# Kernel tuning notes

Measured on AMD Instinct MI355X. Metric: run time of the kernel, lower is better.

Reference implementation:

```python
import jax, jax.numpy as jnp
import numpy as np

S = 10        # spiking_segment_count
TEMP = 50.0

def setup_inputs() -> dict:
    key = jax.random.key(0)
    ks = jax.random.split(key, 6)
    bs, din, dout = 2048, 1024, 1024
    x = jax.random.normal(ks[0], (bs, din), dtype=jnp.float32)
    t = jax.random.uniform(ks[1], (bs,), dtype=jnp.float32)  # in [0,1) subset of [-1,1]
    scale = 1.0 / np.sqrt(din)
    param_W = jax.random.normal(ks[2], (din, dout * S * 3), dtype=jnp.float32) * scale
    param_b = jax.random.normal(ks[3], (dout * S * 3,), dtype=jnp.float32) * 0.01
    norm_W = jax.random.normal(ks[4], (din, dout), dtype=jnp.float32) * scale
    norm_b = jax.random.normal(ks[5], (dout,), dtype=jnp.float32) * 0.01
    return {"x": x, "t": t, "param_W": param_W, "param_b": param_b,
            "norm_W": norm_W, "norm_b": norm_b}

def reference(x, t, param_W, param_b, norm_W, norm_b):
    bs = x.shape[0]
    dout = norm_W.shape[1]
    # param GEMM -> (bs, S, dout, 3)
    params = (x @ param_W + param_b).reshape(bs, S, dout, 3)
    weights = jax.nn.softmax(params[..., 0], axis=1)                 # (bs, S, dout)
    keypoints = jnp.concatenate(
        [jnp.zeros_like(weights[:, :1]), jnp.cumsum(weights, axis=1)], axis=1
    ) * 2.0 - 1.0                                                    # (bs, S+1, dout)
    slopes = jnp.tanh(params[..., 1])
    intercepts = params[..., 2]
    tt = t.reshape(-1, 1, 1)                                         # (bs, 1, 1)
    starts = keypoints[:, :S]
    ends = keypoints[:, 1:]
    residual = slopes * tt + intercepts                              # (bs, S, dout)
    validity = ((tt >= starts) & (tt < ends)) | ((tt == 1.0) & (ends == 1.0))
    vf = validity.astype(x.dtype)
    left_margin = jnp.sum((tt - starts) * vf, axis=1)                # (bs, dout)
    right_margin = jnp.sum((ends - tt) * vf, axis=1)
    lw = jax.nn.sigmoid(-TEMP * left_margin)
    rw = jax.nn.sigmoid(-TEMP * right_margin)
    lv = jnp.concatenate([vf[:, :1], vf[:, :-1]], axis=1)
    rv = jnp.concatenate([vf[:, 1:], vf[:, -1:]], axis=1)
    sw = -(lw + rw - 1.0)
    result = (lw * jnp.sum(residual * lv, axis=1)
              + sw * jnp.sum(residual * vf, axis=1)
              + rw * jnp.sum(residual * rv, axis=1))
    # norm == 'constant': subtract segment-wise integral, add norm_net(x)
    integral = jnp.sum(0.5 * slopes * (ends * ends - starts * starts)
                       + intercepts * weights, axis=1) * 0.5
    norm_target = x @ norm_W + norm_b
    return result - integral + norm_target
```

## Files before the change

### kernel.cpp

```cpp
#include <hip/hip_runtime.h>
#include <cstdint>
#include <cstddef>

#define BS    2048
#define DIN   1024
#define DOUT  1024
#define SSEG  10
#define NPAR  30720
#define NPK   20480
#define NCOL2 21504
#define NLG   10240
#define TAU   5e-5f
#define WL_CAP 1048576u

#define NB_SPLIT 2048
#define NB_NORM  1024
#define NB_TRW   2560

#define GEMM_BLKS 992

typedef _Float16 half_t;
typedef __attribute__((ext_vector_type(8))) _Float16 half8;
typedef __attribute__((ext_vector_type(4))) _Float16 half4;
typedef __attribute__((ext_vector_type(2))) _Float16 half2v;
typedef __attribute__((ext_vector_type(4))) float   floatx4;

__device__ __forceinline__ void gload16(const void* g, void* l) {
  __builtin_amdgcn_global_load_lds(
      (const __attribute__((address_space(1))) void*)g,
      (__attribute__((address_space(3))) void*)l, 16, 0, 0);
}

__global__ void k_zero(unsigned* c) { if (threadIdx.x == 0) *c = 0; }

__global__ __launch_bounds__(256) void k_prep(const float* __restrict__ x,
                                              half_t* __restrict__ xh,
                                              half_t* __restrict__ xl,
                                              const float* __restrict__ nW,
                                              const float* __restrict__ pW,
                                              half_t* __restrict__ wsm,
                                              half_t* __restrict__ wh,
                                              half_t* __restrict__ wlo,
                                              float* __restrict__ wlt,
                                              unsigned* __restrict__ cnt) {
  __shared__ float tile[32][384];
  int bid = blockIdx.x;
  int tid = threadIdx.x;

  if (bid < NB_SPLIT) {
    if (bid == 0 && tid == 0) *cnt = 0;
    int i = bid * 256 + tid;
    floatx4 v = ((const floatx4*)x)[i];
    half4 h, l;
    #pragma unroll
    for (int c = 0; c < 4; c++) { h[c] = (half_t)v[c]; l[c] = (half_t)(v[c] - (float)h[c]); }
    ((half4*)xh)[i] = h;
    ((half4*)xl)[i] = l;
    return;
  }

  if (bid < NB_SPLIT + NB_NORM) {
    int b2 = bid - NB_SPLIT;
    int col0 = (b2 & 31) * 32;
    int k0   = (b2 >> 5) * 32;
    int tx = tid & 31;
    int ty = tid >> 5;
    float* t33 = &tile[0][0];
    #pragma unroll
    for (int r = ty; r < 32; r += 8)
      t33[r * 33 + tx] = nW[(size_t)(k0 + r) * DOUT + col0 + tx];
    __syncthreads();
    #pragma unroll
    for (int r = ty; r < 32; r += 8)
      wsm[(size_t)(col0 + r + NPK) * DIN + k0 + tx] = (half_t)t33[tx * 33 + r];
    return;
  }

  int b3 = bid - NB_SPLIT - NB_NORM;
  int bx = b3 % 80;
  int k0 = (b3 / 80) * 32;
  int s  = bx >> 3;
  int d0 = (bx & 7) * 128;

  const float* sb = pW + (size_t)k0 * NPAR + bx * 384;
  for (int i = tid; i < 32 * 96; i += 256) {
    int r = i / 96, q = i - r * 96;
    ((floatx4*)&tile[r][0])[q] = ((const floatx4*)(sb + (size_t)r * NPAR))[q];
  }
  __syncthreads();

  for (int ci = tid; ci < 3072; ci += 256) {
    if (ci < 1024) {
      int rl = ci >> 2, kc = ci & 3;
      int jj = rl >> 1, cbit = rl & 1;
      int col = 3 * jj + 1 + cbit;
      half8 v;
      #pragma unroll
      for (int m = 0; m < 8; m++) v[m] = (half_t)tile[kc * 8 + m][col];
      *(half8*)(wsm + (size_t)(s * 2048 + 2 * (d0 + jj) + cbit) * DIN + k0 + kc * 8) = v;
    } else if (ci < 1536) {
      int u = ci - 1024;
      int jj = u >> 2, kc = u & 3;
      half8 v;
      #pragma unroll
      for (int m = 0; m < 8; m++) v[m] = (half_t)(tile[kc * 8 + m][3 * jj] * 32.0f);
      *(half8*)(wh + (size_t)(s * 1024 + d0 + jj) * DIN + k0 + kc * 8) = v;
    } else if (ci < 2048) {
      int u = ci - 1536;
      int jj = u >> 2, kc = u & 3;
      half8 v;
      #pragma unroll
      for (int m = 0; m < 8; m++) {
        float raw = tile[kc * 8 + m][3 * jj] * 32.0f;
        half_t h = (half_t)raw;
        v[m] = (half_t)(raw - (float)h);
      }
      *(half8*)(wlo + (size_t)(s * 1024 + d0 + jj) * DIN + k0 + kc * 8) = v;
    } else {
      int u = ci - 2048;
      int jj = u >> 3, kc = u & 7;
      floatx4 v;
      #pragma unroll
      for (int m = 0; m < 4; m++) v[m] = tile[kc * 4 + m][3 * jj];
      *(floatx4*)(wlt + (size_t)(s * 1024 + d0 + jj) * DIN + k0 + kc * 4) = v;
    }
  }
}

__global__ __launch_bounds__(512, 2) void k_gemm2(
    const half_t* __restrict__ xh, const half_t* __restrict__ xl,
    const half_t* __restrict__ wh, const half_t* __restrict__ wlo,
    const half_t* __restrict__ wsm,
    float* __restrict__ Lg, half_t* __restrict__ P,
    const float* __restrict__ pb, const float* __restrict__ nb) {
  __shared__ __attribute__((aligned(128))) char lds[131072];
  char* ldsA = lds;
  char* ldsB = lds + 65536;

  int bid = blockIdx.x;
  int tid = threadIdx.x;
  int w = tid >> 6, l = tid & 63;
  int wr = w >> 2, wc = w & 3;
  int l15 = l & 15, quad = l >> 4;

  int mode, mt, nt, KT;
  const half_t *A0, *A1, *A2, *B0, *B1, *B2;
  if (bid < 320) {
    int s = (bid & 7) * 40 + (bid >> 3);
    mode = 0; mt = s & 7; nt = s >> 3; KT = 96;
    A0 = xh; A1 = xl; A2 = xh; B0 = wh; B1 = wh; B2 = wlo;
  } else {
    int s2 = bid - 320;
    int s = (s2 & 7) * 84 + (s2 >> 3);
    mode = 1; mt = s & 7; nt = s >> 3; KT = 32;
    A0 = xh; A1 = xh; A2 = xh; B0 = wsm; B1 = wsm; B2 = wsm;
  }
  int m0 = mt * 256, n0 = nt * 256;

  int sp = (l & 7) ^ ((l >> 3) & 7);
  int srowA = m0 + w * 32 + 2 * (l >> 3) + (sp >> 2);
  int srowB = n0 + w * 32 + 2 * (l >> 3) + (sp >> 2);
  int scol = (sp & 3) * 8;

  int lofs = (l15 >> 1) * 128 + (((((l15 & 1) << 2) | quad) ^ (l15 >> 1)) << 4);
  const char* pA = ldsA + wr * 8192 + lofs;
  const char* pB = ldsB + wc * 4096 + lofs;

  auto stA = [&](int kt) {
    const half_t* As = (kt < 32) ? A0 : ((kt < 64) ? A1 : A2);
    const half_t* g = As + (size_t)srowA * DIN + (kt & 31) * 32 + scol;
    char* lb = ldsA + (kt & 3) * 16384 + w * 2048;
    gload16(g, lb);
    gload16(g + 16 * DIN, lb + 1024);
  };
  auto stB = [&](int kt) {
    const half_t* Bs = (kt < 32) ? B0 : ((kt < 64) ? B1 : B2);
    const half_t* g = Bs + (size_t)srowB * DIN + (kt & 31) * 32 + scol;
    char* lb = ldsB + (kt & 3) * 16384 + w * 2048;
    gload16(g, lb);
    gload16(g + 16 * DIN, lb + 1024);
  };

  floatx4 acc[8][4] = {};

  stA(0); stB(0); stA(1); stB(1); stA(2); stB(2);
  asm volatile("s_waitcnt vmcnt(8)" ::: "memory");
  __builtin_amdgcn_s_barrier();

  for (int kt = 0; kt < KT; ++kt) {
    const char* a = pA + (kt & 3) * 16384;
    const char* b = pB + (kt & 3) * 16384;
    half8 af[4], bf[4];
    #pragma unroll
    for (int ni = 0; ni < 4; ni++) bf[ni] = *(const half8*)(b + ni * 1024);
    #pragma unroll
    for (int mi = 0; mi < 4; mi++) af[mi] = *(const half8*)(a + mi * 1024);
    if (kt + 3 < KT) stA(kt + 3);
    __builtin_amdgcn_s_barrier();
    asm volatile("s_waitcnt lgkmcnt(0)" ::: "memory");
    __builtin_amdgcn_sched_barrier(0);
    __builtin_amdgcn_s_setprio(1);
    #pragma unroll
    for (int mi = 0; mi < 4; mi++)
      #pragma unroll
      for (int ni = 0; ni < 4; ni++)
        acc[mi][ni] = __builtin_amdgcn_mfma_f32_16x16x32_f16(af[mi], bf[ni], acc[mi][ni], 0, 0, 0);
    __builtin_amdgcn_s_setprio(0);
    __builtin_amdgcn_s_barrier();

    #pragma unroll
    for (int mi = 0; mi < 4; mi++) af[mi] = *(const half8*)(a + 4096 + mi * 1024);
    if (kt + 3 < KT) stB(kt + 3);
    __builtin_amdgcn_s_barrier();
    asm volatile("s_waitcnt lgkmcnt(0)" ::: "memory");
    __builtin_amdgcn_sched_barrier(0);
    __builtin_amdgcn_s_setprio(1);
    #pragma unroll
    for (int mi = 0; mi < 4; mi++)
      #pragma unroll
      for (int ni = 0; ni < 4; ni++)
        acc[4 + mi][ni] = __builtin_amdgcn_mfma_f32_16x16x32_f16(af[mi], bf[ni], acc[4 + mi][ni], 0, 0, 0);
    __builtin_amdgcn_s_setprio(0);
    if (kt < KT - 3)       { asm volatile("s_waitcnt vmcnt(8)" ::: "memory"); }
    else if (kt == KT - 3) { asm volatile("s_waitcnt vmcnt(4)" ::: "memory"); }
    else if (kt == KT - 2) { asm volatile("s_waitcnt vmcnt(0)" ::: "memory"); }
    __builtin_amdgcn_s_barrier();
  }

  int rbase = m0 + wr * 128 + quad * 4;
  int cbase = n0 + wc * 64 + l15;
  if (mode == 0) {
    #pragma unroll
    for (int ni = 0; ni < 4; ni++) {
      int col = cbase + ni * 16;
      float bias = pb[(col >> 10) * 3072 + (col & 1023) * 3];
      #pragma unroll
      for (int mi = 0; mi < 8; mi++) {
        int row = rbase + mi * 16;
        floatx4 v = acc[mi][ni];
        #pragma unroll
        for (int r = 0; r < 4; r++)
          Lg[(size_t)(row + r) * NLG + col] = v[r] * 0.03125f + bias;
      }
    }
  } else {
    #pragma unroll
    for (int ni = 0; ni < 4; ni++) {
      int col = cbase + ni * 16;
      float bias;
      if (col < NPK) {
        int s = col >> 11, rem = col & 2047;
        bias = pb[s * 3072 + 3 * (rem >> 1) + 1 + (rem & 1)];
      } else {
        bias = nb[col - NPK];
      }
      #pragma unroll
      for (int mi = 0; mi < 8; mi++) {
        int row = rbase + mi * 16;
        floatx4 v = acc[mi][ni];
        #pragma unroll
        for (int r = 0; r < 4; r++)
          P[(size_t)(row + r) * NCOL2 + col] = (half_t)(v[r] + bias);
      }
    }
  }
}

__device__ __forceinline__ float spiking_eval(const float* p, float tt, float* mind) {
  float mx = -1e30f;
  #pragma unroll
  for (int s = 0; s < SSEG; s++) mx = fmaxf(mx, p[3 * s]);
  float ew[10], wsum = 0.0f;
  #pragma unroll
  for (int s = 0; s < SSEG; s++) { ew[s] = __expf(p[3 * s] - mx); wsum += ew[s]; }
  float inv = 1.0f / wsum;

  float kp[11];
  kp[0] = -1.0f;
  float cum = 0.0f, md = 1e30f;
  #pragma unroll
  for (int s = 0; s < SSEG; s++) {
    cum += ew[s] * inv;
    kp[s + 1] = cum * 2.0f - 1.0f;
    md = fminf(md, fabsf(tt - kp[s + 1]));
  }
  *mind = md;

  float vf[10], resid[10];
  float lm = 0.0f, rm = 0.0f, integ = 0.0f;
  #pragma unroll
  for (int s = 0; s < SSEG; s++) {
    float p1 = p[3 * s + 1], p2 = p[3 * s + 2];
    float e2 = __expf(2.0f * fabsf(p1));
    float th = copysignf(1.0f - 2.0f / (e2 + 1.0f), p1);
    resid[s] = th * tt + p2;
    float st = kp[s], en = kp[s + 1];
    bool v = ((tt >= st) && (tt < en)) || ((tt == 1.0f) && (en == 1.0f));
    float vv = v ? 1.0f : 0.0f;
    vf[s] = vv;
    lm += (tt - st) * vv;
    rm += (en - tt) * vv;
    integ += 0.5f * th * (en * en - st * st) + p2 * (ew[s] * inv);
  }
  float resLV = 0.0f, resV = 0.0f, resRV = 0.0f;
  #pragma unroll
  for (int s = 0; s < SSEG; s++) {
    float lv = (s == 0) ? vf[0] : vf[s - 1];
    float rv = (s == 9) ? vf[9] : vf[s + 1];
    resLV += resid[s] * lv;
    resV  += resid[s] * vf[s];
    resRV += resid[s] * rv;
  }
  float lw = 1.0f / (1.0f + __expf(50.0f * lm));
  float rw = 1.0f / (1.0f + __expf(50.0f * rm));
  float swt = 1.0f - lw - rw;
  return lw * resLV + swt * resV + rw * resRV - 0.5f * integ + p[30];
}

__global__ __launch_bounds__(256) void k_pointwise(const half_t* __restrict__ P,
                                                   const float* __restrict__ Lg,
                                                   const float* __restrict__ t,
                                                   float* __restrict__ out,
                                                   unsigned* __restrict__ cnt,
                                                   unsigned* __restrict__ wl,
                                                   unsigned cap) {
  __shared__ __attribute__((aligned(16))) half_t sp[SSEG * 512];
  int b = blockIdx.x, dg = blockIdx.y, tid = threadIdx.x;
  const half_t* Pb = P + (size_t)b * NCOL2;
  for (int i = tid; i < SSEG * 64; i += 256) {
    int s = i >> 6, e = i & 63;
    ((uint4*)sp)[(s << 6) + e] = ((const uint4*)(Pb + s * 2048 + dg * 512))[e];
  }
  float tt = t[b];
  float nt = (float)Pb[NPK + dg * 256 + tid];
  const float* Lb = Lg + (size_t)b * NLG + dg * 256 + tid;
  __syncthreads();

  float p[31];
  #pragma unroll
  for (int s = 0; s < SSEG; s++) {
    p[3 * s] = Lb[s * 1024];
    half2v hv = ((const half2v*)sp)[s * 256 + tid];
    p[3 * s + 1] = (float)hv.x;
    p[3 * s + 2] = (float)hv.y;
  }
  p[30] = nt;
  float mind;
  float r = spiking_eval(p, tt, &mind);
  int d = dg * 256 + tid;
  out[(size_t)b * DOUT + d] = r;
  if (wl != nullptr && mind < TAU) {
    unsigned idx = atomicAdd(cnt, 1u);
    if (idx < cap) wl[idx] = ((unsigned)b << 10) | (unsigned)d;
  }
}

__global__ __launch_bounds__(256) void k_naive(const float* __restrict__ x,
                                               const float* __restrict__ t,
                                               const float* __restrict__ pW,
                                               const float* __restrict__ pb,
                                               const float* __restrict__ nW,
                                               const float* __restrict__ nb,
                                               float* __restrict__ out,
                                               unsigned* __restrict__ cnt,
                                               unsigned* __restrict__ wl,
                                               unsigned cap) {
  __shared__ float xs[DIN];
  int b = blockIdx.x, dg = blockIdx.y, tid = threadIdx.x;
  for (int i = tid; i < DIN; i += 256) xs[i] = x[(size_t)b * DIN + i];
  __syncthreads();
  int d = dg * 256 + tid;
  float acc[31];
  #pragma unroll
  for (int i = 0; i < 31; i++) acc[i] = 0.0f;
  for (int k = 0; k < DIN; k++) {
    float xv = xs[k];
    const float* wr = pW + (size_t)k * NPAR + 3 * d;
    #pragma unroll
    for (int s = 0; s < SSEG; s++) {
      acc[3 * s]     += xv * wr[s * 3072];
      acc[3 * s + 1] += xv * wr[s * 3072 + 1];
      acc[3 * s + 2] += xv * wr[s * 3072 + 2];
    }
    acc[30] += xv * nW[(size_t)k * DOUT + d];
  }
  #pragma unroll
  for (int s = 0; s < SSEG; s++) {
    acc[3 * s]     += pb[s * 3072 + 3 * d];
    acc[3 * s + 1] += pb[s * 3072 + 3 * d + 1];
    acc[3 * s + 2] += pb[s * 3072 + 3 * d + 2];
  }
  acc[30] += nb[d];
  float mind;
  float r = spiking_eval(acc, t[b], &mind);
  out[(size_t)b * DOUT + d] = r;
  if (wl != nullptr && mind < TAU) {
    unsigned idx = atomicAdd(cnt, 1u);
    if (idx < cap) wl[idx] = ((unsigned)b << 10) | (unsigned)d;
  }
}

__global__ __launch_bounds__(256) void k_redo(const float* __restrict__ x,
                                              const float* __restrict__ t,
                                              const float* __restrict__ pW,
                                              const float* __restrict__ pb,
                                              const float* __restrict__ nW,
                                              const float* __restrict__ nb,
                                              const half_t* __restrict__ P,
                                              const float* __restrict__ WLt,
                                              int haveP,
                                              const unsigned* __restrict__ cnt,
                                              const unsigned* __restrict__ wl,
                                              unsigned cap,
                                              float* __restrict__ out) {
  unsigned n = *cnt;
  if (n > cap) n = cap;
  int lane = threadIdx.x & 63;
  unsigned wave = (blockIdx.x * 256 + threadIdx.x) >> 6;
  unsigned nwaves = (gridDim.x * 256) >> 6;

  for (unsigned e = wave; e < n; e += nwaves) {
    unsigned code = wl[e];
    int b = (int)(code >> 10), d = (int)(code & 1023);

    double lg[10], sl[10], ic[10], nt = 0.0;
    #pragma unroll
    for (int s = 0; s < SSEG; s++) { lg[s] = 0.0; sl[s] = 0.0; ic[s] = 0.0; }

    if (haveP) {
      for (int k = lane; k < DIN; k += 64) {
        double xv = (double)x[(size_t)b * DIN + k];
        #pragma unroll
        for (int s = 0; s < SSEG; s++)
          lg[s] += xv * (double)WLt[(size_t)(s * 1024 + d) * DIN + k];
      }
    } else {
      for (int k = lane; k < DIN; k += 64) {
        double xv = (double)x[(size_t)b * DIN + k];
        const float* wr = pW + (size_t)k * NPAR + 3 * d;
        #pragma unroll
        for (int s = 0; s < SSEG; s++) {
          lg[s] += xv * (double)wr[s * 3072];
          sl[s] += xv * (double)wr[s * 3072 + 1];
          ic[s] += xv * (double)wr[s * 3072 + 2];
        }
        nt += xv * (double)nW[(size_t)k * DOUT + d];
      }
    }
    #pragma unroll
    for (int off = 32; off > 0; off >>= 1) {
      #pragma unroll
      for (int s = 0; s < SSEG; s++) lg[s] += __shfl_down(lg[s], off);
      if (!haveP) {
        #pragma unroll
        for (int s = 0; s < SSEG; s++) {
          sl[s] += __shfl_down(sl[s], off);
          ic[s] += __shfl_down(ic[s], off);
        }
        nt += __shfl_down(nt, off);
      }
    }

    if (lane == 0) {
      double slope[10], icpt[10], ntv;
      if (haveP) {
        const half_t* Pr = P + (size_t)b * NCOL2;
        #pragma unroll
        for (int s = 0; s < SSEG; s++) {
          slope[s] = tanh((double)(float)Pr[s * 2048 + 2 * d]);
          icpt[s]  = (double)(float)Pr[s * 2048 + 2 * d + 1];
        }
        ntv = (double)(float)Pr[NPK + d];
      } else {
        #pragma unroll
        for (int s = 0; s < SSEG; s++) {
          slope[s] = tanh(sl[s] + (double)pb[s * 3072 + 3 * d + 1]);
          icpt[s]  = ic[s] + (double)pb[s * 3072 + 3 * d + 2];
        }
        ntv = nt + (double)nb[d];
      }
      #pragma unroll
      for (int s = 0; s < SSEG; s++) lg[s] += (double)pb[s * 3072 + 3 * d];

      double mx = -1e300;
      #pragma unroll
      for (int s = 0; s < SSEG; s++) mx = fmax(mx, lg[s]);
      double ew[10], ws = 0.0;
      #pragma unroll
      for (int s = 0; s < SSEG; s++) { ew[s] = exp(lg[s] - mx); ws += ew[s]; }

      double kp[11];
      kp[0] = -1.0;
      double cum = 0.0;
      #pragma unroll
      for (int s = 0; s < SSEG; s++) { cum += ew[s] / ws; kp[s + 1] = cum * 2.0 - 1.0; }

      double tt = (double)t[b];
      double vf[10], resid[10], lm = 0.0, rm = 0.0, integ = 0.0;
      #pragma unroll
      for (int s = 0; s < SSEG; s++) {
        double st = kp[s], en = kp[s + 1];
        bool v = ((tt >= st) && (tt < en)) || ((tt == 1.0) && (en == 1.0));
        double vv = v ? 1.0 : 0.0;
        vf[s] = vv;
        resid[s] = slope[s] * tt + icpt[s];
        lm += (tt - st) * vv;
        rm += (en - tt) * vv;
        integ += 0.5 * slope[s] * (en * en - st * st) + icpt[s] * (ew[s] / ws);
      }
      double rLV = 0.0, rV = 0.0, rRV = 0.0;
      #pragma unroll
      for (int s = 0; s < SSEG; s++) {
        double lv = (s == 0) ? vf[0] : vf[s - 1];
        double rv = (s == 9) ? vf[9] : vf[s + 1];
        rLV += resid[s] * lv;
        rV  += resid[s] * vf[s];
        rRV += resid[s] * rv;
      }
      double lw = 1.0 / (1.0 + exp(50.0 * lm));
      double rw = 1.0 / (1.0 + exp(50.0 * rm));
      double res = lw * rLV + (1.0 - lw - rw) * rV + rw * rRV - 0.5 * integ + ntv;
      out[(size_t)b * DOUT + d] = (float)res;
    }
  }
}

extern "C" void kernel_launch(void* const* d_in, const int* in_sizes, int n_in,
                              void* d_out, int out_size, void* d_ws, size_t ws_size,
                              hipStream_t stream) {
  const float* x  = (const float*)d_in[0];
  const float* t  = (const float*)d_in[1];
  const float* pW = (const float*)d_in[2];
  const float* pb = (const float*)d_in[3];
  const float* nW = (const float*)d_in[4];
  const float* nb = (const float*)d_in[5];
  float* out = (float*)d_out;

  const size_t o_cnt = 0;
  const size_t o_wl  = 64;
  const size_t o_xh  = o_wl  + (size_t)WL_CAP * 4;
  const size_t o_xl  = o_xh  + (size_t)BS * DIN * 2;
  const size_t o_wsm = o_xl  + (size_t)BS * DIN * 2;
  const size_t o_wh  = o_wsm + (size_t)NCOL2 * DIN * 2;
  const size_t o_wlo = o_wh  + (size_t)NLG * DIN * 2;
  const size_t o_wlt = o_wlo + (size_t)NLG * DIN * 2;
  const size_t o_p   = o_wlt + (size_t)NLG * DIN * 4;
  const size_t o_lg  = o_p   + (size_t)BS * NCOL2 * 2;
  const size_t need  = o_lg  + (size_t)BS * NLG * 4;

  bool have_wl = ws_size >= 1024 * 1024;
  unsigned* cnt = (unsigned*)((char*)d_ws + o_cnt);
  unsigned* wl  = (unsigned*)((char*)d_ws + o_wl);
  unsigned cap  = 0;
  if (have_wl) {
    size_t avail = (ws_size >= need) ? (size_t)WL_CAP
                                     : (ws_size - o_wl) / 4;
    cap = (unsigned)(avail < WL_CAP ? avail : WL_CAP);
  }

  if (ws_size >= need) {
    half_t* xh  = (half_t*)((char*)d_ws + o_xh);
    half_t* xl  = (half_t*)((char*)d_ws + o_xl);
    half_t* wsm = (half_t*)((char*)d_ws + o_wsm);
    half_t* wh  = (half_t*)((char*)d_ws + o_wh);
    half_t* wlo = (half_t*)((char*)d_ws + o_wlo);
    float*  wlt = (float*)((char*)d_ws + o_wlt);
    half_t* P   = (half_t*)((char*)d_ws + o_p);
    float*  Lg  = (float*)((char*)d_ws + o_lg);

    k_prep<<<NB_SPLIT + NB_NORM + NB_TRW, 256, 0, stream>>>(x, xh, xl, nW, pW,
                                                            wsm, wh, wlo, wlt, cnt);
    k_gemm2<<<GEMM_BLKS, 512, 0, stream>>>(xh, xl, wh, wlo, wsm, Lg, P, pb, nb);
    k_pointwise<<<dim3(BS, DOUT / 256), 256, 0, stream>>>(P, Lg, t, out, cnt,
                                                          have_wl ? wl : nullptr, cap);
    if (have_wl)
      k_redo<<<256, 256, 0, stream>>>(x, t, pW, pb, nW, nb, P, wlt, 1, cnt, wl, cap, out);
  } else {
    if (have_wl) k_zero<<<1, 64, 0, stream>>>(cnt);
    k_naive<<<dim3(BS, DOUT / 256), 256, 0, stream>>>(x, t, pW, pb, nW, nb, out, cnt,
                                                      have_wl ? wl : nullptr, cap);
    if (have_wl)
      k_redo<<<256, 256, 0, stream>>>(x, t, pW, pb, nW, nb, nullptr, nullptr, 0,
                                      cnt, wl, cap, out);
  }
}
```

Before: 561.2 us.

## Fuse three split-precision GEMM passes into one K loop sharing staged tiles

```diff
diff --git a/kernel.cpp b/kernel.cpp
--- a/kernel.cpp
+++ b/kernel.cpp
@@ -134,8 +134,6 @@
     float* __restrict__ Lg, half_t* __restrict__ P,
     const float* __restrict__ pb, const float* __restrict__ nb) {
   __shared__ __attribute__((aligned(128))) char lds[131072];
-  char* ldsA = lds;
-  char* ldsB = lds + 65536;
 
   int bid = blockIdx.x;
   int tid = threadIdx.x;
@@ -143,18 +141,9 @@
   int wr = w >> 2, wc = w & 3;
   int l15 = l & 15, quad = l >> 4;
 
-  int mode, mt, nt, KT;
-  const half_t *A0, *A1, *A2, *B0, *B1, *B2;
-  if (bid < 320) {
-    int s = (bid & 7) * 40 + (bid >> 3);
-    mode = 0; mt = s & 7; nt = s >> 3; KT = 96;
-    A0 = xh; A1 = xl; A2 = xh; B0 = wh; B1 = wh; B2 = wlo;
-  } else {
-    int s2 = bid - 320;
-    int s = (s2 & 7) * 84 + (s2 >> 3);
-    mode = 1; mt = s & 7; nt = s >> 3; KT = 32;
-    A0 = xh; A1 = xh; A2 = xh; B0 = wsm; B1 = wsm; B2 = wsm;
-  }
+  int mode, mt, nt;
+  if (bid < 320) { mode = 0; mt = bid & 7; nt = bid >> 3; }
+  else { int s2 = bid - 320; mode = 1; mt = s2 & 7; nt = s2 >> 3; }
   int m0 = mt * 256, n0 = nt * 256;
 
   int sp = (l & 7) ^ ((l >> 3) & 7);
@@ -163,68 +152,121 @@
   int scol = (sp & 3) * 8;
 
   int lofs = (l15 >> 1) * 128 + (((((l15 & 1) << 2) | quad) ^ (l15 >> 1)) << 4);
-  const char* pA = ldsA + wr * 8192 + lofs;
-  const char* pB = ldsB + wc * 4096 + lofs;
-
-  auto stA = [&](int kt) {
-    const half_t* As = (kt < 32) ? A0 : ((kt < 64) ? A1 : A2);
-    const half_t* g = As + (size_t)srowA * DIN + (kt & 31) * 32 + scol;
-    char* lb = ldsA + (kt & 3) * 16384 + w * 2048;
-    gload16(g, lb);
-    gload16(g + 16 * DIN, lb + 1024);
-  };
-  auto stB = [&](int kt) {
-    const half_t* Bs = (kt < 32) ? B0 : ((kt < 64) ? B1 : B2);
-    const half_t* g = Bs + (size_t)srowB * DIN + (kt & 31) * 32 + scol;
-    char* lb = ldsB + (kt & 3) * 16384 + w * 2048;
-    gload16(g, lb);
-    gload16(g + 16 * DIN, lb + 1024);
-  };
 
   floatx4 acc[8][4] = {};
 
-  stA(0); stB(0); stA(1); stB(1); stA(2); stB(2);
-  asm volatile("s_waitcnt vmcnt(8)" ::: "memory");
-  __builtin_amdgcn_s_barrier();
-
-  for (int kt = 0; kt < KT; ++kt) {
-    const char* a = pA + (kt & 3) * 16384;
-    const char* b = pB + (kt & 3) * 16384;
-    half8 af[4], bf[4];
-    #pragma unroll
-    for (int ni = 0; ni < 4; ni++) bf[ni] = *(const half8*)(b + ni * 1024);
-    #pragma unroll
-    for (int mi = 0; mi < 4; mi++) af[mi] = *(const half8*)(a + mi * 1024);
-    if (kt + 3 < KT) stA(kt + 3);
+  if (mode == 0) {
+    auto stage0 = [&](int c) {
+      char* base = lds + ((c & 1) * 65536) + w * 2048;
+      const half_t* ga = xh + (size_t)srowA * DIN + c * 32 + scol;
+      const half_t* gx = xl + (size_t)srowA * DIN + c * 32 + scol;
+      const half_t* gh = wh + (size_t)srowB * DIN + c * 32 + scol;
+      const half_t* gl = wlo + (size_t)srowB * DIN + c * 32 + scol;
+      gload16(ga, base);                gload16(ga + 16 * DIN, base + 1024);
+      gload16(gx, base + 16384);        gload16(gx + 16 * DIN, base + 16384 + 1024);
+      gload16(gh, base + 32768);        gload16(gh + 16 * DIN, base + 32768 + 1024);
+      gload16(gl, base + 49152);        gload16(gl + 16 * DIN, base + 49152 + 1024);
+    };
+
+    stage0(0);
+    asm volatile("s_waitcnt vmcnt(0)" ::: "memory");
     __builtin_amdgcn_s_barrier();
-    asm volatile("s_waitcnt lgkmcnt(0)" ::: "memory");
-    __builtin_amdgcn_sched_barrier(0);
-    __builtin_amdgcn_s_setprio(1);
-    #pragma unroll
-    for (int mi = 0; mi < 4; mi++)
-      #pragma unroll
-      for (int ni = 0; ni < 4; ni++)
-        acc[mi][ni] = __builtin_amdgcn_mfma_f32_16x16x32_f16(af[mi], bf[ni], acc[mi][ni], 0, 0, 0);
-    __builtin_amdgcn_s_setprio(0);
+
+    for (int c = 0; c < 32; ++c) {
+      const char* base = lds + (c & 1) * 65536;
+      const char* aXH = base + wr * 8192 + lofs;
+      const char* aXL = base + 16384 + wr * 8192 + lofs;
+      const char* bWH = base + 32768 + wc * 4096 + lofs;
+      const char* bWL = base + 49152 + wc * 4096 + lofs;
+      if (c + 1 < 32) stage0(c + 1);
+
+      half8 bh[4], bl[4], a0[4], a1[4], x0[4], x1[4];
+      #pragma unroll
+      for (int ni = 0; ni < 4; ni++) bh[ni] = *(const half8*)(bWH + ni * 1024);
+      #pragma unroll
+      for (int mi = 0; mi < 4; mi++) a0[mi] = *(const half8*)(aXH + mi * 1024);
+      #pragma unroll
+      for (int mi = 0; mi < 4; mi++) a1[mi] = *(const half8*)(aXH + 4096 + mi * 1024);
+      #pragma unroll
+      for (int mi = 0; mi < 4; mi++)
+        #pragma unroll
+        for (int ni = 0; ni < 4; ni++) {
+          acc[mi][ni]     = __builtin_amdgcn_mfma_f32_16x16x32_f16(a0[mi], bh[ni], acc[mi][ni], 0, 0, 0);
+          acc[4 + mi][ni] = __builtin_amdgcn_mfma_f32_16x16x32_f16(a1[mi], bh[ni], acc[4 + mi][ni], 0, 0, 0);
+        }
+      #pragma unroll
+      for (int mi = 0; mi < 4; mi++) x0[mi] = *(const half8*)(aXL + mi * 1024);
+      #pragma unroll
+      for (int mi = 0; mi < 4; mi++) x1[mi] = *(const half8*)(aXL + 4096 + mi * 1024);
+      #pragma unroll
+      for (int mi = 0; mi < 4; mi++)
+        #pragma unroll
+        for (int ni = 0; ni < 4; ni++) {
+          acc[mi][ni]     = __builtin_amdgcn_mfma_f32_16x16x32_f16(x0[mi], bh[ni], acc[mi][ni], 0, 0, 0);
+          acc[4 + mi][ni] = __builtin_amdgcn_mfma_f32_16x16x32_f16(x1[mi], bh[ni], acc[4 + mi][ni], 0, 0, 0);
+        }
+      #pragma unroll
+      for (int ni = 0; ni < 4; ni++) bl[ni] = *(const half8*)(bWL + ni * 1024);
+      #pragma unroll
+      for (int mi = 0; mi < 4; mi++)
+        #pragma unroll
+        for (int ni = 0; ni < 4; ni++) {
+          acc[mi][ni]     = __builtin_amdgcn_mfma_f32_16x16x32_f16(a0[mi], bl[ni], acc[mi][ni], 0, 0, 0);
+          acc[4 + mi][ni] = __builtin_amdgcn_mfma_f32_16x16x32_f16(a1[mi], bl[ni], acc[4 + mi][ni], 0, 0, 0);
+        }
+      if (c + 1 < 32) {
+        __builtin_amdgcn_sched_barrier(0);
+        asm volatile("s_waitcnt vmcnt(0)" ::: "memory");
+        __builtin_amdgcn_s_barrier();
+      }
+    }
+  } else {
+    auto stage1 = [&](int kt) {
+      char* base = lds + ((kt & 3) * 32768) + w * 2048;
+      const half_t* ga = xh + (size_t)srowA * DIN + kt * 32 + scol;
+      const half_t* gb = wsm + (size_t)srowB * DIN + kt * 32 + scol;
+      gload16(ga, base);            gload16(ga + 16 * DIN, base + 1024);
+      gload16(gb, base + 16384);    gload16(gb + 16 * DIN, base + 16384 + 1024);
+    };
+
+    stage1(0); stage1(1); stage1(2);
+    asm volatile("s_waitcnt vmcnt(8)" ::: "memory");
     __builtin_amdgcn_s_barrier();
 
-    #pragma unroll
-    for (int mi = 0; mi < 4; mi++) af[mi] = *(const half8*)(a + 4096 + mi * 1024);
-    if (kt + 3 < KT) stB(kt + 3);
-    __builtin_amdgcn_s_barrier();
-    asm volatile("s_waitcnt lgkmcnt(0)" ::: "memory");
-    __builtin_amdgcn_sched_barrier(0);
-    __builtin_amdgcn_s_setprio(1);
-    #pragma unroll
-    for (int mi = 0; mi < 4; mi++)
-      #pragma unroll
-      for (int ni = 0; ni < 4; ni++)
-        acc[4 + mi][ni] = __builtin_amdgcn_mfma_f32_16x16x32_f16(af[mi], bf[ni], acc[4 + mi][ni], 0, 0, 0);
-    __builtin_amdgcn_s_setprio(0);
-    if (kt < KT - 3)       { asm volatile("s_waitcnt vmcnt(8)" ::: "memory"); }
-    else if (kt == KT - 3) { asm volatile("s_waitcnt vmcnt(4)" ::: "memory"); }
-    else if (kt == KT - 2) { asm volatile("s_waitcnt vmcnt(0)" ::: "memory"); }
-    __builtin_amdgcn_s_barrier();
+    for (int kt = 0; kt < 32; ++kt) {
+      const char* base = lds + (kt & 3) * 32768;
+      const char* a = base + wr * 8192 + lofs;
+      const char* b = base + 16384 + wc * 4096 + lofs;
+      if (kt + 3 < 32) stage1(kt + 3);
+
+      half8 bf[4], af[4], ag[4];
+      #pragma unroll
+      for (int ni = 0; ni < 4; ni++) bf[ni] = *(const half8*)(b + ni * 1024);
+      #pragma unroll
+      for (int mi = 0; mi < 4; mi++) af[mi] = *(const half8*)(a + mi * 1024);
+      #pragma unroll
+      for (int mi = 0; mi < 4; mi++) ag[mi] = *(const half8*)(a + 4096 + mi * 1024);
+      #pragma unroll
+      for (int mi = 0; mi < 4; mi++)
+        #pragma unroll
+        for (int ni = 0; ni < 4; ni++) {
+          acc[mi][ni]     = __builtin_amdgcn_mfma_f32_16x16x32_f16(af[mi], bf[ni], acc[mi][ni], 0, 0, 0);
+          acc[4 + mi][ni] = __builtin_amdgcn_mfma_f32_16x16x32_f16(ag[mi], bf[ni], acc[4 + mi][ni], 0, 0, 0);
+        }
+      if (kt < 29) {
+        __builtin_amdgcn_sched_barrier(0);
+        asm volatile("s_waitcnt vmcnt(8)" ::: "memory");
+        __builtin_amdgcn_s_barrier();
+      } else if (kt == 29) {
+        __builtin_amdgcn_sched_barrier(0);
+        asm volatile("s_waitcnt vmcnt(4)" ::: "memory");
+        __builtin_amdgcn_s_barrier();
+      } else if (kt == 30) {
+        __builtin_amdgcn_sched_barrier(0);
+        asm volatile("s_waitcnt vmcnt(0)" ::: "memory");
+        __builtin_amdgcn_s_barrier();
+      }
+    }
   }
 
   int rbase = m0 + wr * 128 + quad * 4;
```

Result: no change. 565.7 us (+0.8%).
